# Kernel tuning notes

Measured on AMD Instinct MI355X. Metric: run time of the kernel, lower is better.

Reference implementation:

```python
import jax, jax.numpy as jnp
import numpy as np

SEGMENT_LENGTHS = [2048, 4096, 8192]
DILATION_RATES = [1, 2, 4]
BATCH, SEQ_LEN, HEADS, HEAD_DIM = 1, 8192, 16, 64
SCALE = HEAD_DIM ** (-0.5)


def _hilbert_index_to_xy(index, n):
    # Exact replica of the torch module's integer Hilbert d->(x,y) mapping.
    x = y = 0
    s = 1
    while s < n:
        rx = 1 & (index // 2)
        ry = 1 & (index ^ rx)
        if ry == 0:
            if rx == 1:
                x, y = s - 1 - y, s - 1 - x
            x, y = y, x
        x += s * rx
        y += s * ry
        index //= 4
        s *= 2
    return x, y


def _hilbert_perm(n):
    # Replicates _generate_hilbert_indices, including the fill-in tail and
    d = 1
    while d * d < n:
        d *= 2
    idx = []
    for i in range(min(n, d * d)):
        x, y = _hilbert_index_to_xy(i, d)
        p = x * d + y
        if p < n:
            idx.append(p)
    if len(idx) < n:
        idx.extend(range(len(idx), n))
    perm = np.array(idx[:n], dtype=np.int64)
    inv = np.zeros(n, dtype=np.int64)
    inv[perm] = np.arange(n, dtype=np.int64)
    return perm, inv


_PERM_CACHE = {}


def _get_perm(n):
    if n not in _PERM_CACHE:
        _PERM_CACHE[n] = _hilbert_perm(n)
    return _PERM_CACHE[n]


def setup_inputs() -> dict:
    key = jax.random.key(0)
    kq, kk, kv = jax.random.split(key, 3)
    shape = (BATCH, SEQ_LEN, HEADS, HEAD_DIM)
    return {
        "q": jax.random.normal(kq, shape, dtype=jnp.float32),
        "k": jax.random.normal(kk, shape, dtype=jnp.float32),
        "v": jax.random.normal(kv, shape, dtype=jnp.float32),
    }


def reference(q, k, v) -> jnp.ndarray:
    B, L, H, D = q.shape
    n_groups = len(SEGMENT_LENGTHS)
    heads_per_group = max(1, H // n_groups)
    out = jnp.zeros_like(q)
    for g, (seg_len, dil) in enumerate(zip(SEGMENT_LENGTHS, DILATION_RATES)):
        S = min(seg_len, L)
        h0 = g * heads_per_group
        if h0 >= H:
            continue
        h1 = min(h0 + heads_per_group, H)
        assert L % S == 0, "seq_len must tile into segments"
        N = L // S  # number of segments
        Hg = h1 - h0
        # [B, N, S, Hg, D]
        qg = q[:, :, h0:h1].reshape(B, N, S, Hg, D)
        kg = k[:, :, h0:h1].reshape(B, N, S, Hg, D)
        vg = v[:, :, h0:h1].reshape(B, N, S, Hg, D)
        if S > 64:
            perm, inv = _get_perm(S)
        else:
            perm = np.arange(S, dtype=np.int64)
            inv = perm
        # dilation applied AFTER Hilbert ordering -> compose the gathers
        kv_idx = perm[np.arange(0, S, dil)]
        qp = qg[:, :, perm]           # [B,N,S,Hg,D]
        kd = kg[:, :, kv_idx]         # [B,N,S/dil,Hg,D]
        vd = vg[:, :, kv_idx]
        scores = jnp.einsum('bnqhd,bnkhd->bnhqk', qp, kd) * SCALE
        attn = jnp.nan_to_num(jax.nn.softmax(scores, axis=-1))
        og = jnp.einsum('bnhqk,bnkhd->bnqhd', attn, vd)  # [B,N,S,Hg,D]
        og = og[:, :, inv]            # inverse Hilbert scatter
        out = out.at[:, :, h0:h1].set(og.reshape(B, L, Hg, D))
    return out
```

## Files before the change

### kernel.cpp

```cpp
#include <hip/hip_runtime.h>
#include <hip/hip_bf16.h>

typedef __attribute__((ext_vector_type(8))) short bf16x8;
typedef __attribute__((ext_vector_type(16))) float f32x16;
typedef __attribute__((ext_vector_type(2))) unsigned u32x2;

__device__ __forceinline__ unsigned pk2(float a, float b) {
    union { __hip_bfloat162 h2; unsigned u; } c;
    c.h2 = __float22bfloat162_rn(make_float2(a, b));
    return c.u;
}

__device__ __forceinline__ void gld16(const void* g, void* l) {
    __builtin_amdgcn_global_load_lds(
        (const __attribute__((address_space(1))) unsigned*)g,
        (__attribute__((address_space(3))) unsigned*)l, 16, 0, 0);
}

__device__ inline int hilbert_p(int index, int d) {
    int x = 0, y = 0;
    for (int s = 1; s < d; s <<= 1) {
        int rx = (index >> 1) & 1;
        int ry = (index ^ rx) & 1;
        if (ry == 0) {
            if (rx == 1) {
                int nx = s - 1 - y;
                int ny = s - 1 - x;
                x = nx; y = ny;
            }
            int t = x; x = y; y = t;
        }
        x += s * rx;
        y += s * ry;
        index >>= 2;
    }
    return x * d + y;
}

struct TileGeo { int g, h, segrow, dgrid, kt; };
__device__ __forceinline__ TileGeo tile_decode(int b) {
    TileGeo t;
    int g, rb;
    if (b < 640)      { g = 0; rb = b; }
    else if (b < 960) { g = 1; rb = b - 640; }
    else              { g = 2; rb = b - 960; }
    const int nseg = 4 >> g;
    const int hl   = rb / (nseg * 32);
    const int r2   = rb - hl * (nseg * 32);
    t.g      = g;
    t.h      = g * 5 + hl;
    t.kt     = r2 & 31;
    t.segrow = (r2 >> 5) * (2048 << g);
    t.dgrid  = (g == 2) ? 128 : 64;
    return t;
}

__device__ __forceinline__ void k_item(int i, const float* __restrict__ K,
                                       short* __restrict__ Kp) {
    const int tile = i >> 9, idx = i & 511;
    const int j = idx >> 3, c8 = idx & 7;
    const TileGeo t = tile_decode(tile);
    const int ii = t.kt * 64 + j;
    const int p  = (t.g == 0) ? ii : hilbert_p(ii << t.g, t.dgrid);
    const float* kp = K + ((size_t)((t.segrow + p) * 16 + t.h)) * 64 + c8 * 8;
    float4 k0 = ((const float4*)kp)[0];
    float4 k1 = ((const float4*)kp)[1];
    union { unsigned u4[4]; bf16x8 v; } ck;
    ck.u4[0] = pk2(k0.x, k0.y); ck.u4[1] = pk2(k0.z, k0.w);
    ck.u4[2] = pk2(k1.x, k1.y); ck.u4[3] = pk2(k1.z, k1.w);
    const int kchunk = ((j >> 5) * 4 + (c8 >> 1)) * 64 + (c8 & 1) * 32 + (j & 31);
    *(bf16x8*)&Kp[(size_t)tile * 4096 + kchunk * 8] = ck.v;
}

__device__ __forceinline__ void v_item(int i, const float* __restrict__ V,
                                       short* __restrict__ Vp) {
    const int tile = i >> 9, idx = i & 511;
    const int k8 = idx >> 6, dd = idx & 63;
    const TileGeo t = tile_decode(tile);
    float rv[8];
#pragma unroll
    for (int u = 0; u < 8; ++u) {
        const int ii = t.kt * 64 + k8 * 8 + u;
        const int p  = (t.g == 0) ? ii : hilbert_p(ii << t.g, t.dgrid);
        rv[u] = V[((size_t)((t.segrow + p) * 16 + t.h)) * 64 + dd];
    }
    union { unsigned u4[4]; bf16x8 v; } o;
    o.u4[0] = pk2(rv[0], rv[1]); o.u4[1] = pk2(rv[2], rv[3]);
    o.u4[2] = pk2(rv[4], rv[5]); o.u4[3] = pk2(rv[6], rv[7]);
    const int vchunk = ((k8 >> 1) * 2 + (dd >> 5)) * 64 + (k8 & 1) * 32 + (dd & 31);
    *(bf16x8*)&Vp[(size_t)tile * 4096 + vchunk * 8] = o.v;
}

__global__ __launch_bounds__(256, 4) void gather_kv(
    const float* __restrict__ K, const float* __restrict__ V,
    short* __restrict__ Kp, short* __restrict__ Vp)
{
    const int gt   = blockIdx.x * 256 + threadIdx.x;
    const int step = gridDim.x * 256;
    for (int i = gt; i < 1120 * 512; i += step) k_item(i, K, Kp);
    for (int i = gt; i < 1120 * 512; i += step) v_item(i, V, Vp);
}

__global__ __launch_bounds__(256, 4) void attn_kernel(
    const float* __restrict__ Q, float* __restrict__ O,
    const short* __restrict__ Kp, const short* __restrict__ Vp)
{
    __shared__ __align__(16) short ldsK[2][4096];
    __shared__ __align__(16) short ldsV[2][4096];

    const int bx = blockIdx.x;
    const int g  = bx / 320;
    const int r  = bx - g * 320;
    const int hl = r >> 6;
    const int qb = r & 63;
    const int h  = g * 5 + hl;
    const int qglob = qb * 128;
    const int seg   = qb >> (4 + g);
    const int tile0 = ((g == 0) ? 0 : (g == 1) ? 640 : 960) + (hl * (4 >> g) + seg) * 32;

    const int tid  = threadIdx.x;
    const int wave = tid >> 6;
    const int lane = tid & 63;
    const int l31  = lane & 31;
    const int hi   = lane >> 5;

    if (g == 0 && hl == 0) {
        const float4 z = make_float4(0.f, 0.f, 0.f, 0.f);
        for (int i = tid; i < 2048; i += 256) {
            int row = qglob + (i >> 4);
            ((float4*)O)[(size_t)(row * 16 + 15) * 16 + (i & 15)] = z;
        }
    }

    const float cs = 0.125f * 1.44269504088896f;
    bf16x8 qf[4];
    {
        const int qrow = qglob + wave * 32 + l31;
        const float* qp = Q + ((size_t)(qrow * 16 + h)) * 64;
#pragma unroll
        for (int ks = 0; ks < 4; ++ks) {
            const float4* p4 = (const float4*)(qp + ks * 16 + hi * 8);
            float4 a = p4[0], b = p4[1];
            union { unsigned u[4]; bf16x8 v; } f;
            f.u[0] = pk2(a.x * cs, a.y * cs); f.u[1] = pk2(a.z * cs, a.w * cs);
            f.u[2] = pk2(b.x * cs, b.y * cs); f.u[3] = pk2(b.z * cs, b.w * cs);
            qf[ks] = f.v;
        }
    }

    f32x16 z16;
#pragma unroll
    for (int rr = 0; rr < 16; ++rr) z16[rr] = 0.f;

    f32x16 oacc[2];
    oacc[0] = z16; oacc[1] = z16;
    float lp = 0.f;

    const int lbase = lane * 8;

    {
        const size_t tb = (size_t)tile0 << 13;
        const char* kgp = (const char*)Kp + tb + (wave << 11) + (lane << 4);
        const char* vgp = (const char*)Vp + tb + (wave << 11) + (lane << 4);
        char* klp = (char*)&ldsK[0][0] + (wave << 11);
        char* vlp = (char*)&ldsV[0][0] + (wave << 11);
        gld16(kgp,        klp);
        gld16(kgp + 1024, klp + 1024);
        gld16(vgp,        vlp);
        gld16(vgp + 1024, vlp + 1024);
    }

    for (int kt = 0; kt < 32; ++kt) {
        const int cur = kt & 1;

        asm volatile("s_waitcnt vmcnt(0)" ::: "memory");
        asm volatile("s_barrier" ::: "memory");

        if (kt < 31) {
            const size_t tb = (size_t)(tile0 + kt + 1) << 13;
            const char* kgp = (const char*)Kp + tb + (wave << 11) + (lane << 4);
            const char* vgp = (const char*)Vp + tb + (wave << 11) + (lane << 4);
            char* klp = (char*)&ldsK[cur ^ 1][0] + (wave << 11);
            char* vlp = (char*)&ldsV[cur ^ 1][0] + (wave << 11);
            gld16(kgp,        klp);
            gld16(kgp + 1024, klp + 1024);
            gld16(vgp,        vlp);
            gld16(vgp + 1024, vlp + 1024);
        }

        const short* lK = &ldsK[cur][lbase];
        const short* lV = &ldsV[cur][lbase];

        float lacc = 0.f;
        unsigned dw[16];
        __builtin_amdgcn_s_setprio(1);
#pragma unroll
        for (int kb = 0; kb < 2; ++kb) {
            bf16x8 kf0 = *(const bf16x8*)&lK[(kb * 4 + 0) * 512];
            bf16x8 kf1 = *(const bf16x8*)&lK[(kb * 4 + 1) * 512];
            bf16x8 kf2 = *(const bf16x8*)&lK[(kb * 4 + 2) * 512];
            bf16x8 kf3 = *(const bf16x8*)&lK[(kb * 4 + 3) * 512];
            f32x16 sa;
            sa = __builtin_amdgcn_mfma_f32_32x32x16_bf16(kf0, qf[0], z16, 0, 0, 0);
            sa = __builtin_amdgcn_mfma_f32_32x32x16_bf16(kf1, qf[1], sa, 0, 0, 0);
            sa = __builtin_amdgcn_mfma_f32_32x32x16_bf16(kf2, qf[2], sa, 0, 0, 0);
            sa = __builtin_amdgcn_mfma_f32_32x32x16_bf16(kf3, qf[3], sa, 0, 0, 0);
            float pe[16];
#pragma unroll
            for (int rr = 0; rr < 16; ++rr) pe[rr] = __builtin_amdgcn_exp2f(sa[rr]);
            lacc += (((pe[0] + pe[1]) + (pe[2] + pe[3])) + ((pe[4] + pe[5]) + (pe[6] + pe[7])))
                  + (((pe[8] + pe[9]) + (pe[10] + pe[11])) + ((pe[12] + pe[13]) + (pe[14] + pe[15])));
#pragma unroll
            for (int kslo = 0; kslo < 2; ++kslo)
#pragma unroll
                for (int j = 0; j < 2; ++j)
#pragma unroll
                    for (int hT = 0; hT < 2; ++hT) {
                        const int r0 = 2 * j + 8 * kslo + 4 * hT;
                        dw[(kb * 2 + kslo) * 4 + j * 2 + hT] = pk2(pe[r0], pe[r0 + 1]);
                    }
        }
        __builtin_amdgcn_s_setprio(0);
        lp += lacc;

        bf16x8 pa[4];
#pragma unroll
        for (int ks = 0; ks < 4; ++ks) {
            u32x2 r0 = __builtin_amdgcn_permlane32_swap(dw[ks * 4 + 0], dw[ks * 4 + 1], false, false);
            u32x2 r1 = __builtin_amdgcn_permlane32_swap(dw[ks * 4 + 2], dw[ks * 4 + 3], false, false);
            union { unsigned u[4]; bf16x8 v; } p;
            p.u[0] = r0[0]; p.u[1] = r1[0]; p.u[2] = r0[1]; p.u[3] = r1[1];
            pa[ks] = p.v;
        }

        __builtin_amdgcn_sched_barrier(0);

        bf16x8 vf[4][2];
#pragma unroll
        for (int ks = 0; ks < 4; ++ks)
#pragma unroll
            for (int db = 0; db < 2; ++db)
                vf[ks][db] = *(const bf16x8*)&lV[(ks * 2 + db) * 512];

        __builtin_amdgcn_s_setprio(1);
#pragma unroll
        for (int ks = 0; ks < 4; ++ks) {
            oacc[0] = __builtin_amdgcn_mfma_f32_32x32x16_bf16(pa[ks], vf[ks][0], oacc[0], 0, 0, 0);
            oacc[1] = __builtin_amdgcn_mfma_f32_32x32x16_bf16(pa[ks], vf[ks][1], oacc[1], 0, 0, 0);
        }
        __builtin_amdgcn_s_setprio(0);
    }

    float ltot = lp + __shfl_xor(lp, 32, 64);
    float linv = 1.0f / ltot;

#pragma unroll
    for (int rr = 0; rr < 16; ++rr) {
        const int m = (rr & 3) + ((rr >> 2) << 3) + (hi << 2);
        float inv = __shfl(linv, m, 64);
        const int qrow = qglob + wave * 32 + m;
        float* op = O + ((size_t)(qrow * 16 + h)) * 64 + l31;
        op[0]  = oacc[0][rr] * inv;
        op[32] = oacc[1][rr] * inv;
    }
}

extern "C" void kernel_launch(void* const* d_in, const int* in_sizes, int n_in,
                              void* d_out, int out_size, void* d_ws, size_t ws_size,
                              hipStream_t stream) {
    const float* q = (const float*)d_in[0];
    const float* k = (const float*)d_in[1];
    const float* v = (const float*)d_in[2];
    float* out = (float*)d_out;
    short* Kp = (short*)d_ws;
    short* Vp = Kp + (size_t)1120 * 4096;

    gather_kv<<<960, 256, 0, stream>>>(k, v, Kp, Vp);
    attn_kernel<<<960, 256, 0, stream>>>(q, out, Kp, Vp);
}
```

Baseline: 209.2 us.

## Process two 32-row query tiles per wave with 128-thread blocks

Each block now uses 2 waves instead of 4, and each wave handles 64 query rows as two 32-row sub-tiles. Each K/V fragment read from LDS feeds two MFMAs, halving LDS reads per FLOP and giving more independent MFMA chains for latency hiding. Each wave now issues twice as many global-to-LDS loads per tile. The trade-off is higher register pressure and half as many waves per block, which may lower occupancy and latency hiding.

```diff
diff --git a/kernel.cpp b/kernel.cpp
--- a/kernel.cpp
+++ b/kernel.cpp
@@ -101,7 +101,7 @@
     for (int i = gt; i < 1120 * 512; i += step) v_item(i, V, Vp);
 }
 
-__global__ __launch_bounds__(256, 4) void attn_kernel(
+__global__ __launch_bounds__(128, 2) void attn_kernel(
     const float* __restrict__ Q, float* __restrict__ O,
     const short* __restrict__ Kp, const short* __restrict__ Vp)
 {
@@ -126,16 +126,17 @@
 
     if (g == 0 && hl == 0) {
         const float4 z = make_float4(0.f, 0.f, 0.f, 0.f);
-        for (int i = tid; i < 2048; i += 256) {
+        for (int i = tid; i < 2048; i += 128) {
             int row = qglob + (i >> 4);
             ((float4*)O)[(size_t)(row * 16 + 15) * 16 + (i & 15)] = z;
         }
     }
 
     const float cs = 0.125f * 1.44269504088896f;
-    bf16x8 qf[4];
-    {
-        const int qrow = qglob + wave * 32 + l31;
+    bf16x8 qfA[4], qfB[4];
+#pragma unroll
+    for (int qs = 0; qs < 2; ++qs) {
+        const int qrow = qglob + wave * 64 + qs * 32 + l31;
         const float* qp = Q + ((size_t)(qrow * 16 + h)) * 64;
 #pragma unroll
         for (int ks = 0; ks < 4; ++ks) {
@@ -144,7 +145,7 @@
             union { unsigned u[4]; bf16x8 v; } f;
             f.u[0] = pk2(a.x * cs, a.y * cs); f.u[1] = pk2(a.z * cs, a.w * cs);
             f.u[2] = pk2(b.x * cs, b.y * cs); f.u[3] = pk2(b.z * cs, b.w * cs);
-            qf[ks] = f.v;
+            if (qs == 0) qfA[ks] = f.v; else qfB[ks] = f.v;
         }
     }
 
@@ -152,22 +153,21 @@
 #pragma unroll
     for (int rr = 0; rr < 16; ++rr) z16[rr] = 0.f;
 
-    f32x16 oacc[2];
-    oacc[0] = z16; oacc[1] = z16;
-    float lp = 0.f;
+    f32x16 oaccA0 = z16, oaccA1 = z16, oaccB0 = z16, oaccB1 = z16;
+    float lpA = 0.f, lpB = 0.f;
 
     const int lbase = lane * 8;
 
     {
         const size_t tb = (size_t)tile0 << 13;
-        const char* kgp = (const char*)Kp + tb + (wave << 11) + (lane << 4);
-        const char* vgp = (const char*)Vp + tb + (wave << 11) + (lane << 4);
-        char* klp = (char*)&ldsK[0][0] + (wave << 11);
-        char* vlp = (char*)&ldsV[0][0] + (wave << 11);
-        gld16(kgp,        klp);
-        gld16(kgp + 1024, klp + 1024);
-        gld16(vgp,        vlp);
-        gld16(vgp + 1024, vlp + 1024);
+        const char* kgp = (const char*)Kp + tb + (wave << 12) + (lane << 4);
+        const char* vgp = (const char*)Vp + tb + (wave << 12) + (lane << 4);
+        char* klp = (char*)&ldsK[0][0] + (wave << 12);
+        char* vlp = (char*)&ldsV[0][0] + (wave << 12);
+        gld16(kgp,        klp);        gld16(kgp + 1024, klp + 1024);
+        gld16(kgp + 2048, klp + 2048); gld16(kgp + 3072, klp + 3072);
+        gld16(vgp,        vlp);        gld16(vgp + 1024, vlp + 1024);
+        gld16(vgp + 2048, vlp + 2048); gld16(vgp + 3072, vlp + 3072);
     }
 
     for (int kt = 0; kt < 32; ++kt) {
@@ -178,21 +178,21 @@
 
         if (kt < 31) {
             const size_t tb = (size_t)(tile0 + kt + 1) << 13;
-            const char* kgp = (const char*)Kp + tb + (wave << 11) + (lane << 4);
-            const char* vgp = (const char*)Vp + tb + (wave << 11) + (lane << 4);
-            char* klp = (char*)&ldsK[cur ^ 1][0] + (wave << 11);
-            char* vlp = (char*)&ldsV[cur ^ 1][0] + (wave << 11);
-            gld16(kgp,        klp);
-            gld16(kgp + 1024, klp + 1024);
-            gld16(vgp,        vlp);
-            gld16(vgp + 1024, vlp + 1024);
+            const char* kgp = (const char*)Kp + tb + (wave << 12) + (lane << 4);
+            const char* vgp = (const char*)Vp + tb + (wave << 12) + (lane << 4);
+            char* klp = (char*)&ldsK[cur ^ 1][0] + (wave << 12);
+            char* vlp = (char*)&ldsV[cur ^ 1][0] + (wave << 12);
+            gld16(kgp,        klp);        gld16(kgp + 1024, klp + 1024);
+            gld16(kgp + 2048, klp + 2048); gld16(kgp + 3072, klp + 3072);
+            gld16(vgp,        vlp);        gld16(vgp + 1024, vlp + 1024);
+            gld16(vgp + 2048, vlp + 2048); gld16(vgp + 3072, vlp + 3072);
         }
 
         const short* lK = &ldsK[cur][lbase];
         const short* lV = &ldsV[cur][lbase];
 
-        float lacc = 0.f;
-        unsigned dw[16];
+        float laccA = 0.f, laccB = 0.f;
+        unsigned dwA[16], dwB[16];
         __builtin_amdgcn_s_setprio(1);
 #pragma unroll
         for (int kb = 0; kb < 2; ++kb) {
@@ -200,16 +200,25 @@
             bf16x8 kf1 = *(const bf16x8*)&lK[(kb * 4 + 1) * 512];
             bf16x8 kf2 = *(const bf16x8*)&lK[(kb * 4 + 2) * 512];
             bf16x8 kf3 = *(const bf16x8*)&lK[(kb * 4 + 3) * 512];
-            f32x16 sa;
-            sa = __builtin_amdgcn_mfma_f32_32x32x16_bf16(kf0, qf[0], z16, 0, 0, 0);
-            sa = __builtin_amdgcn_mfma_f32_32x32x16_bf16(kf1, qf[1], sa, 0, 0, 0);
-            sa = __builtin_amdgcn_mfma_f32_32x32x16_bf16(kf2, qf[2], sa, 0, 0, 0);
-            sa = __builtin_amdgcn_mfma_f32_32x32x16_bf16(kf3, qf[3], sa, 0, 0, 0);
-            float pe[16];
-#pragma unroll
-            for (int rr = 0; rr < 16; ++rr) pe[rr] = __builtin_amdgcn_exp2f(sa[rr]);
-            lacc += (((pe[0] + pe[1]) + (pe[2] + pe[3])) + ((pe[4] + pe[5]) + (pe[6] + pe[7])))
-                  + (((pe[8] + pe[9]) + (pe[10] + pe[11])) + ((pe[12] + pe[13]) + (pe[14] + pe[15])));
+            f32x16 sa0, sa1;
+            sa0 = __builtin_amdgcn_mfma_f32_32x32x16_bf16(kf0, qfA[0], z16, 0, 0, 0);
+            sa1 = __builtin_amdgcn_mfma_f32_32x32x16_bf16(kf0, qfB[0], z16, 0, 0, 0);
+            sa0 = __builtin_amdgcn_mfma_f32_32x32x16_bf16(kf1, qfA[1], sa0, 0, 0, 0);
+            sa1 = __builtin_amdgcn_mfma_f32_32x32x16_bf16(kf1, qfB[1], sa1, 0, 0, 0);
+            sa0 = __builtin_amdgcn_mfma_f32_32x32x16_bf16(kf2, qfA[2], sa0, 0, 0, 0);
+            sa1 = __builtin_amdgcn_mfma_f32_32x32x16_bf16(kf2, qfB[2], sa1, 0, 0, 0);
+            sa0 = __builtin_amdgcn_mfma_f32_32x32x16_bf16(kf3, qfA[3], sa0, 0, 0, 0);
+            sa1 = __builtin_amdgcn_mfma_f32_32x32x16_bf16(kf3, qfB[3], sa1, 0, 0, 0);
+
+            float peA[16], peB[16];
+#pragma unroll
+            for (int rr = 0; rr < 16; ++rr) peA[rr] = __builtin_amdgcn_exp2f(sa0[rr]);
+#pragma unroll
+            for (int rr = 0; rr < 16; ++rr) peB[rr] = __builtin_amdgcn_exp2f(sa1[rr]);
+            laccA += (((peA[0] + peA[1]) + (peA[2] + peA[3])) + ((peA[4] + peA[5]) + (peA[6] + peA[7])))
+                   + (((peA[8] + peA[9]) + (peA[10] + peA[11])) + ((peA[12] + peA[13]) + (peA[14] + peA[15])));
+            laccB += (((peB[0] + peB[1]) + (peB[2] + peB[3])) + ((peB[4] + peB[5]) + (peB[6] + peB[7])))
+                   + (((peB[8] + peB[9]) + (peB[10] + peB[11])) + ((peB[12] + peB[13]) + (peB[14] + peB[15])));
 #pragma unroll
             for (int kslo = 0; kslo < 2; ++kslo)
 #pragma unroll
@@ -217,20 +226,25 @@
 #pragma unroll
                     for (int hT = 0; hT < 2; ++hT) {
                         const int r0 = 2 * j + 8 * kslo + 4 * hT;
-                        dw[(kb * 2 + kslo) * 4 + j * 2 + hT] = pk2(pe[r0], pe[r0 + 1]);
+                        const int di = (kb * 2 + kslo) * 4 + j * 2 + hT;
+                        dwA[di] = pk2(peA[r0], peA[r0 + 1]);
+                        dwB[di] = pk2(peB[r0], peB[r0 + 1]);
                     }
         }
         __builtin_amdgcn_s_setprio(0);
-        lp += lacc;
-
-        bf16x8 pa[4];
+        lpA += laccA; lpB += laccB;
+
+        bf16x8 paA[4], paB[4];
 #pragma unroll
         for (int ks = 0; ks < 4; ++ks) {
-            u32x2 r0 = __builtin_amdgcn_permlane32_swap(dw[ks * 4 + 0], dw[ks * 4 + 1], false, false);
-            u32x2 r1 = __builtin_amdgcn_permlane32_swap(dw[ks * 4 + 2], dw[ks * 4 + 3], false, false);
-            union { unsigned u[4]; bf16x8 v; } p;
-            p.u[0] = r0[0]; p.u[1] = r1[0]; p.u[2] = r0[1]; p.u[3] = r1[1];
-            pa[ks] = p.v;
+            u32x2 a0 = __builtin_amdgcn_permlane32_swap(dwA[ks * 4 + 0], dwA[ks * 4 + 1], false, false);
+            u32x2 a1 = __builtin_amdgcn_permlane32_swap(dwA[ks * 4 + 2], dwA[ks * 4 + 3], false, false);
+            u32x2 b0 = __builtin_amdgcn_permlane32_swap(dwB[ks * 4 + 0], dwB[ks * 4 + 1], false, false);
+            u32x2 b1 = __builtin_amdgcn_permlane32_swap(dwB[ks * 4 + 2], dwB[ks * 4 + 3], false, false);
+            union { unsigned u[4]; bf16x8 v; } pA, pB;
+            pA.u[0] = a0[0]; pA.u[1] = a1[0]; pA.u[2] = a0[1]; pA.u[3] = a1[1];
+            pB.u[0] = b0[0]; pB.u[1] = b1[0]; pB.u[2] = b0[1]; pB.u[3] = b1[1];
+            paA[ks] = pA.v;  paB[ks] = pB.v;
         }
 
         __builtin_amdgcn_sched_barrier(0);
@@ -245,23 +259,32 @@
         __builtin_amdgcn_s_setprio(1);
 #pragma unroll
         for (int ks = 0; ks < 4; ++ks) {
-            oacc[0] = __builtin_amdgcn_mfma_f32_32x32x16_bf16(pa[ks], vf[ks][0], oacc[0], 0, 0, 0);
-            oacc[1] = __builtin_amdgcn_mfma_f32_32x32x16_bf16(pa[ks], vf[ks][1], oacc[1], 0, 0, 0);
+            oaccA0 = __builtin_amdgcn_mfma_f32_32x32x16_bf16(paA[ks], vf[ks][0], oaccA0, 0, 0, 0);
+            oaccB0 = __builtin_amdgcn_mfma_f32_32x32x16_bf16(paB[ks], vf[ks][0], oaccB0, 0, 0, 0);
+            oaccA1 = __builtin_amdgcn_mfma_f32_32x32x16_bf16(paA[ks], vf[ks][1], oaccA1, 0, 0, 0);
+            oaccB1 = __builtin_amdgcn_mfma_f32_32x32x16_bf16(paB[ks], vf[ks][1], oaccB1, 0, 0, 0);
         }
         __builtin_amdgcn_s_setprio(0);
     }
 
-    float ltot = lp + __shfl_xor(lp, 32, 64);
-    float linv = 1.0f / ltot;
+    float ltA = lpA + __shfl_xor(lpA, 32, 64);
+    float ltB = lpB + __shfl_xor(lpB, 32, 64);
+    float invA = 1.0f / ltA;
+    float invB = 1.0f / ltB;
 
 #pragma unroll
     for (int rr = 0; rr < 16; ++rr) {
         const int m = (rr & 3) + ((rr >> 2) << 3) + (hi << 2);
-        float inv = __shfl(linv, m, 64);
-        const int qrow = qglob + wave * 32 + m;
-        float* op = O + ((size_t)(qrow * 16 + h)) * 64 + l31;
-        op[0]  = oacc[0][rr] * inv;
-        op[32] = oacc[1][rr] * inv;
+        float iA = __shfl(invA, m, 64);
+        float iB = __shfl(invB, m, 64);
+        const int qrowA = qglob + wave * 64 + m;
+        const int qrowB = qrowA + 32;
+        float* opA = O + ((size_t)(qrowA * 16 + h)) * 64 + l31;
+        float* opB = O + ((size_t)(qrowB * 16 + h)) * 64 + l31;
+        opA[0]  = oaccA0[rr] * iA;
+        opA[32] = oaccA1[rr] * iA;
+        opB[0]  = oaccB0[rr] * iB;
+        opB[32] = oaccB1[rr] * iB;
     }
 }
 
@@ -276,5 +299,5 @@
     short* Vp = Kp + (size_t)1120 * 4096;
 
     gather_kv<<<960, 256, 0, stream>>>(k, v, Kp, Vp);
-    attn_kernel<<<960, 256, 0, stream>>>(q, out, Kp, Vp);
-}
+    attn_kernel<<<960, 128, 0, stream>>>(q, out, Kp, Vp);
+}
```

Measured after the change: 217.6 us. +4.0%, slower.

## Load K/V tiles directly from global into registers, dropping LDS staging

Applied to the files above, without the earlier changes.

Removes the double-buffered LDS staging of K and V tiles, which used global_load_lds with a barrier every iteration. Each wave now loads its own K and V fragments straight from global memory into registers. The next tile's loads are issued as soon as the current fragments are consumed, so register prefetch replaces the LDS pipeline and the barriers go away. The extra live registers force the occupancy target down from 4 to 3 blocks per CU. The four waves in a block each load the same K/V tile separately, which raises global/L2 traffic.

```diff
diff --git a/kernel.cpp b/kernel.cpp
--- a/kernel.cpp
+++ b/kernel.cpp
@@ -9,12 +9,6 @@
     union { __hip_bfloat162 h2; unsigned u; } c;
     c.h2 = __float22bfloat162_rn(make_float2(a, b));
     return c.u;
-}
-
-__device__ __forceinline__ void gld16(const void* g, void* l) {
-    __builtin_amdgcn_global_load_lds(
-        (const __attribute__((address_space(1))) unsigned*)g,
-        (__attribute__((address_space(3))) unsigned*)l, 16, 0, 0);
 }
 
 __device__ inline int hilbert_p(int index, int d) {
@@ -101,13 +95,10 @@
     for (int i = gt; i < 1120 * 512; i += step) v_item(i, V, Vp);
 }
 
-__global__ __launch_bounds__(256, 4) void attn_kernel(
+__global__ __launch_bounds__(256, 3) void attn_kernel(
     const float* __restrict__ Q, float* __restrict__ O,
     const short* __restrict__ Kp, const short* __restrict__ Vp)
 {
-    __shared__ __align__(16) short ldsK[2][4096];
-    __shared__ __align__(16) short ldsV[2][4096];
-
     const int bx = blockIdx.x;
     const int g  = bx / 320;
     const int r  = bx - g * 320;
@@ -156,55 +147,29 @@
     oacc[0] = z16; oacc[1] = z16;
     float lp = 0.f;
 
-    const int lbase = lane * 8;
-
-    {
-        const size_t tb = (size_t)tile0 << 13;
-        const char* kgp = (const char*)Kp + tb + (wave << 11) + (lane << 4);
-        const char* vgp = (const char*)Vp + tb + (wave << 11) + (lane << 4);
-        char* klp = (char*)&ldsK[0][0] + (wave << 11);
-        char* vlp = (char*)&ldsV[0][0] + (wave << 11);
-        gld16(kgp,        klp);
-        gld16(kgp + 1024, klp + 1024);
-        gld16(vgp,        vlp);
-        gld16(vgp + 1024, vlp + 1024);
-    }
+    const short* kp0 = Kp + ((size_t)tile0 << 12) + lane * 8;
+    const short* vp0 = Vp + ((size_t)tile0 << 12) + lane * 8;
+
+    bf16x8 kf[8], vf[8];
+#pragma unroll
+    for (int i = 0; i < 8; ++i) kf[i] = *(const bf16x8*)&kp0[i * 512];
+#pragma unroll
+    for (int i = 0; i < 8; ++i) vf[i] = *(const bf16x8*)&vp0[i * 512];
 
     for (int kt = 0; kt < 32; ++kt) {
-        const int cur = kt & 1;
-
-        asm volatile("s_waitcnt vmcnt(0)" ::: "memory");
-        asm volatile("s_barrier" ::: "memory");
-
-        if (kt < 31) {
-            const size_t tb = (size_t)(tile0 + kt + 1) << 13;
-            const char* kgp = (const char*)Kp + tb + (wave << 11) + (lane << 4);
-            const char* vgp = (const char*)Vp + tb + (wave << 11) + (lane << 4);
-            char* klp = (char*)&ldsK[cur ^ 1][0] + (wave << 11);
-            char* vlp = (char*)&ldsV[cur ^ 1][0] + (wave << 11);
-            gld16(kgp,        klp);
-            gld16(kgp + 1024, klp + 1024);
-            gld16(vgp,        vlp);
-            gld16(vgp + 1024, vlp + 1024);
-        }
-
-        const short* lK = &ldsK[cur][lbase];
-        const short* lV = &ldsV[cur][lbase];
+        const short* kp_n = kp0 + (size_t)(kt + 1) * 4096;
+        const short* vp_n = vp0 + (size_t)(kt + 1) * 4096;
 
         float lacc = 0.f;
         unsigned dw[16];
         __builtin_amdgcn_s_setprio(1);
 #pragma unroll
         for (int kb = 0; kb < 2; ++kb) {
-            bf16x8 kf0 = *(const bf16x8*)&lK[(kb * 4 + 0) * 512];
-            bf16x8 kf1 = *(const bf16x8*)&lK[(kb * 4 + 1) * 512];
-            bf16x8 kf2 = *(const bf16x8*)&lK[(kb * 4 + 2) * 512];
-            bf16x8 kf3 = *(const bf16x8*)&lK[(kb * 4 + 3) * 512];
             f32x16 sa;
-            sa = __builtin_amdgcn_mfma_f32_32x32x16_bf16(kf0, qf[0], z16, 0, 0, 0);
-            sa = __builtin_amdgcn_mfma_f32_32x32x16_bf16(kf1, qf[1], sa, 0, 0, 0);
-            sa = __builtin_amdgcn_mfma_f32_32x32x16_bf16(kf2, qf[2], sa, 0, 0, 0);
-            sa = __builtin_amdgcn_mfma_f32_32x32x16_bf16(kf3, qf[3], sa, 0, 0, 0);
+            sa = __builtin_amdgcn_mfma_f32_32x32x16_bf16(kf[kb * 4 + 0], qf[0], z16, 0, 0, 0);
+            sa = __builtin_amdgcn_mfma_f32_32x32x16_bf16(kf[kb * 4 + 1], qf[1], sa, 0, 0, 0);
+            sa = __builtin_amdgcn_mfma_f32_32x32x16_bf16(kf[kb * 4 + 2], qf[2], sa, 0, 0, 0);
+            sa = __builtin_amdgcn_mfma_f32_32x32x16_bf16(kf[kb * 4 + 3], qf[3], sa, 0, 0, 0);
             float pe[16];
 #pragma unroll
             for (int rr = 0; rr < 16; ++rr) pe[rr] = __builtin_amdgcn_exp2f(sa[rr]);
@@ -222,6 +187,13 @@
         }
         __builtin_amdgcn_s_setprio(0);
         lp += lacc;
+
+        __builtin_amdgcn_sched_barrier(0);
+        if (kt < 31) {
+#pragma unroll
+            for (int i = 0; i < 8; ++i) kf[i] = *(const bf16x8*)&kp_n[i * 512];
+        }
+        __builtin_amdgcn_sched_barrier(0);
 
         bf16x8 pa[4];
 #pragma unroll
@@ -233,22 +205,20 @@
             pa[ks] = p.v;
         }
 
-        __builtin_amdgcn_sched_barrier(0);
-
-        bf16x8 vf[4][2];
-#pragma unroll
-        for (int ks = 0; ks < 4; ++ks)
-#pragma unroll
-            for (int db = 0; db < 2; ++db)
-                vf[ks][db] = *(const bf16x8*)&lV[(ks * 2 + db) * 512];
-
         __builtin_amdgcn_s_setprio(1);
 #pragma unroll
         for (int ks = 0; ks < 4; ++ks) {
-            oacc[0] = __builtin_amdgcn_mfma_f32_32x32x16_bf16(pa[ks], vf[ks][0], oacc[0], 0, 0, 0);
-            oacc[1] = __builtin_amdgcn_mfma_f32_32x32x16_bf16(pa[ks], vf[ks][1], oacc[1], 0, 0, 0);
+            oacc[0] = __builtin_amdgcn_mfma_f32_32x32x16_bf16(pa[ks], vf[ks * 2 + 0], oacc[0], 0, 0, 0);
+            oacc[1] = __builtin_amdgcn_mfma_f32_32x32x16_bf16(pa[ks], vf[ks * 2 + 1], oacc[1], 0, 0, 0);
         }
         __builtin_amdgcn_s_setprio(0);
+
+        __builtin_amdgcn_sched_barrier(0);
+        if (kt < 31) {
+#pragma unroll
+            for (int i = 0; i < 8; ++i) vf[i] = *(const bf16x8*)&vp_n[i * 512];
+        }
+        __builtin_amdgcn_sched_barrier(0);
     }
 
     float ltot = lp + __shfl_xor(lp, 32, 64);
```

Measured after the change: 219.4 us. +4.9%, slower.

## Software-pipeline PV matmul one tile behind QK and softmax

Applied to the files above, without the earlier changes.

Restructures the key-tile loop so the P·V MFMAs for the previous tile are issued between the two halves of the current tile's QK^T MFMAs. V fragments and packed probabilities are carried in registers across iterations, and an epilogue handles the last tile. The aim is to overlap exp/pack VALU work with matrix-core work, at the cost of more live registers (16 dwords plus 8 bf16x8), which may lower occupancy.

```diff
diff --git a/kernel.cpp b/kernel.cpp
--- a/kernel.cpp
+++ b/kernel.cpp
@@ -158,6 +158,9 @@
 
     const int lbase = lane * 8;
 
+    unsigned dw_prev[16];
+    bf16x8  vf_prev[8];
+
     {
         const size_t tb = (size_t)tile0 << 13;
         const char* kgp = (const char*)Kp + tb + (wave << 11) + (lane << 4);
@@ -191,23 +194,66 @@
         const short* lK = &ldsK[cur][lbase];
         const short* lV = &ldsV[cur][lbase];
 
+        f32x16 sa0;
+        __builtin_amdgcn_s_setprio(1);
+        {
+            bf16x8 k0 = *(const bf16x8*)&lK[0 * 512];
+            bf16x8 k1 = *(const bf16x8*)&lK[1 * 512];
+            bf16x8 k2 = *(const bf16x8*)&lK[2 * 512];
+            bf16x8 k3 = *(const bf16x8*)&lK[3 * 512];
+            sa0 = __builtin_amdgcn_mfma_f32_32x32x16_bf16(k0, qf[0], z16, 0, 0, 0);
+            sa0 = __builtin_amdgcn_mfma_f32_32x32x16_bf16(k1, qf[1], sa0, 0, 0, 0);
+            sa0 = __builtin_amdgcn_mfma_f32_32x32x16_bf16(k2, qf[2], sa0, 0, 0, 0);
+            sa0 = __builtin_amdgcn_mfma_f32_32x32x16_bf16(k3, qf[3], sa0, 0, 0, 0);
+        }
+        __builtin_amdgcn_s_setprio(0);
+        __builtin_amdgcn_sched_barrier(0);
+
+        if (kt > 0) {
+            bf16x8 pa[4];
+#pragma unroll
+            for (int ks = 0; ks < 4; ++ks) {
+                u32x2 r0 = __builtin_amdgcn_permlane32_swap(dw_prev[ks * 4 + 0], dw_prev[ks * 4 + 1], false, false);
+                u32x2 r1 = __builtin_amdgcn_permlane32_swap(dw_prev[ks * 4 + 2], dw_prev[ks * 4 + 3], false, false);
+                union { unsigned u[4]; bf16x8 v; } p;
+                p.u[0] = r0[0]; p.u[1] = r1[0]; p.u[2] = r0[1]; p.u[3] = r1[1];
+                pa[ks] = p.v;
+            }
+            __builtin_amdgcn_s_setprio(1);
+#pragma unroll
+            for (int ks = 0; ks < 4; ++ks) {
+                oacc[0] = __builtin_amdgcn_mfma_f32_32x32x16_bf16(pa[ks], vf_prev[ks * 2 + 0], oacc[0], 0, 0, 0);
+                oacc[1] = __builtin_amdgcn_mfma_f32_32x32x16_bf16(pa[ks], vf_prev[ks * 2 + 1], oacc[1], 0, 0, 0);
+            }
+            __builtin_amdgcn_s_setprio(0);
+        }
+        __builtin_amdgcn_sched_barrier(0);
+
+        f32x16 sa1;
+        __builtin_amdgcn_s_setprio(1);
+        {
+            bf16x8 k0 = *(const bf16x8*)&lK[4 * 512];
+            bf16x8 k1 = *(const bf16x8*)&lK[5 * 512];
+            bf16x8 k2 = *(const bf16x8*)&lK[6 * 512];
+            bf16x8 k3 = *(const bf16x8*)&lK[7 * 512];
+            sa1 = __builtin_amdgcn_mfma_f32_32x32x16_bf16(k0, qf[0], z16, 0, 0, 0);
+            sa1 = __builtin_amdgcn_mfma_f32_32x32x16_bf16(k1, qf[1], sa1, 0, 0, 0);
+            sa1 = __builtin_amdgcn_mfma_f32_32x32x16_bf16(k2, qf[2], sa1, 0, 0, 0);
+            sa1 = __builtin_amdgcn_mfma_f32_32x32x16_bf16(k3, qf[3], sa1, 0, 0, 0);
+        }
+        __builtin_amdgcn_s_setprio(0);
+        __builtin_amdgcn_sched_barrier(0);
+
+#pragma unroll
+        for (int i = 0; i < 8; ++i)
+            vf_prev[i] = *(const bf16x8*)&lV[i * 512];
+        __builtin_amdgcn_sched_barrier(0);
+
         float lacc = 0.f;
-        unsigned dw[16];
-        __builtin_amdgcn_s_setprio(1);
-#pragma unroll
-        for (int kb = 0; kb < 2; ++kb) {
-            bf16x8 kf0 = *(const bf16x8*)&lK[(kb * 4 + 0) * 512];
-            bf16x8 kf1 = *(const bf16x8*)&lK[(kb * 4 + 1) * 512];
-            bf16x8 kf2 = *(const bf16x8*)&lK[(kb * 4 + 2) * 512];
-            bf16x8 kf3 = *(const bf16x8*)&lK[(kb * 4 + 3) * 512];
-            f32x16 sa;
-            sa = __builtin_amdgcn_mfma_f32_32x32x16_bf16(kf0, qf[0], z16, 0, 0, 0);
-            sa = __builtin_amdgcn_mfma_f32_32x32x16_bf16(kf1, qf[1], sa, 0, 0, 0);
-            sa = __builtin_amdgcn_mfma_f32_32x32x16_bf16(kf2, qf[2], sa, 0, 0, 0);
-            sa = __builtin_amdgcn_mfma_f32_32x32x16_bf16(kf3, qf[3], sa, 0, 0, 0);
+        {
             float pe[16];
 #pragma unroll
-            for (int rr = 0; rr < 16; ++rr) pe[rr] = __builtin_amdgcn_exp2f(sa[rr]);
+            for (int rr = 0; rr < 16; ++rr) pe[rr] = __builtin_amdgcn_exp2f(sa0[rr]);
             lacc += (((pe[0] + pe[1]) + (pe[2] + pe[3])) + ((pe[4] + pe[5]) + (pe[6] + pe[7])))
                   + (((pe[8] + pe[9]) + (pe[10] + pe[11])) + ((pe[12] + pe[13]) + (pe[14] + pe[15])));
 #pragma unroll
@@ -217,38 +263,43 @@
 #pragma unroll
                     for (int hT = 0; hT < 2; ++hT) {
                         const int r0 = 2 * j + 8 * kslo + 4 * hT;
-                        dw[(kb * 2 + kslo) * 4 + j * 2 + hT] = pk2(pe[r0], pe[r0 + 1]);
+                        dw_prev[kslo * 4 + j * 2 + hT] = pk2(pe[r0], pe[r0 + 1]);
                     }
         }
-        __builtin_amdgcn_s_setprio(0);
+        {
+            float pe[16];
+#pragma unroll
+            for (int rr = 0; rr < 16; ++rr) pe[rr] = __builtin_amdgcn_exp2f(sa1[rr]);
+            lacc += (((pe[0] + pe[1]) + (pe[2] + pe[3])) + ((pe[4] + pe[5]) + (pe[6] + pe[7])))
+                  + (((pe[8] + pe[9]) + (pe[10] + pe[11])) + ((pe[12] + pe[13]) + (pe[14] + pe[15])));
+#pragma unroll
+            for (int kslo = 0; kslo < 2; ++kslo)
+#pragma unroll
+                for (int j = 0; j < 2; ++j)
+#pragma unroll
+                    for (int hT = 0; hT < 2; ++hT) {
+                        const int r0 = 2 * j + 8 * kslo + 4 * hT;
+                        dw_prev[(2 + kslo) * 4 + j * 2 + hT] = pk2(pe[r0], pe[r0 + 1]);
+                    }
+        }
         lp += lacc;
-
+    }
+
+    {
         bf16x8 pa[4];
 #pragma unroll
         for (int ks = 0; ks < 4; ++ks) {
-            u32x2 r0 = __builtin_amdgcn_permlane32_swap(dw[ks * 4 + 0], dw[ks * 4 + 1], false, false);
-            u32x2 r1 = __builtin_amdgcn_permlane32_swap(dw[ks * 4 + 2], dw[ks * 4 + 3], false, false);
+            u32x2 r0 = __builtin_amdgcn_permlane32_swap(dw_prev[ks * 4 + 0], dw_prev[ks * 4 + 1], false, false);
+            u32x2 r1 = __builtin_amdgcn_permlane32_swap(dw_prev[ks * 4 + 2], dw_prev[ks * 4 + 3], false, false);
             union { unsigned u[4]; bf16x8 v; } p;
             p.u[0] = r0[0]; p.u[1] = r1[0]; p.u[2] = r0[1]; p.u[3] = r1[1];
             pa[ks] = p.v;
         }
-
-        __builtin_amdgcn_sched_barrier(0);
-
-        bf16x8 vf[4][2];
-#pragma unroll
-        for (int ks = 0; ks < 4; ++ks)
-#pragma unroll
-            for (int db = 0; db < 2; ++db)
-                vf[ks][db] = *(const bf16x8*)&lV[(ks * 2 + db) * 512];
-
-        __builtin_amdgcn_s_setprio(1);
 #pragma unroll
         for (int ks = 0; ks < 4; ++ks) {
-            oacc[0] = __builtin_amdgcn_mfma_f32_32x32x16_bf16(pa[ks], vf[ks][0], oacc[0], 0, 0, 0);
-            oacc[1] = __builtin_amdgcn_mfma_f32_32x32x16_bf16(pa[ks], vf[ks][1], oacc[1], 0, 0, 0);
-        }
-        __builtin_amdgcn_s_setprio(0);
+            oacc[0] = __builtin_amdgcn_mfma_f32_32x32x16_bf16(pa[ks], vf_prev[ks * 2 + 0], oacc[0], 0, 0, 0);
+            oacc[1] = __builtin_amdgcn_mfma_f32_32x32x16_bf16(pa[ks], vf_prev[ks * 2 + 1], oacc[1], 0, 0, 0);
+        }
     }
 
     float ltot = lp + __shfl_xor(lp, 32, 64);
```

Result: slower. 238.5 us (+14.0%).
